# Optimization experiments

Hardware: AMD Instinct MI355X
Metric: run time of the kernel (lower is better)

Reference implementation:

```python
import jax, jax.numpy as jnp
import numpy as np

IN_SHAPE = (8, 16, 8)     # hidden_shape, prod = 1024
FF_SHAPE = (16, 16, 16)   # ff_shape, prod = 4096
RANKS = (1, 8, 8, 1)      # tt_ranks


def _make_cores(key, in_shape, out_shape, ranks):
    cores = []
    for k in range(3):
        key, sub = jax.random.split(key)
        shape = (ranks[k], in_shape[k], out_shape[k], ranks[k + 1])
        # glorot-ish scale per core
        scale = (2.0 / (in_shape[k] * ranks[k] + out_shape[k] * ranks[k + 1])) ** 0.5
        cores.append(jax.random.normal(sub, shape, dtype=jnp.float32) * scale)
    return key, cores


def setup_inputs() -> dict:
    key = jax.random.key(0)
    key, kx = jax.random.split(key)
    x = jax.random.normal(kx, (8192, int(np.prod(IN_SHAPE))), dtype=jnp.float32)
    key, c0 = _make_cores(key, IN_SHAPE, FF_SHAPE, RANKS)
    key, c1 = _make_cores(key, FF_SHAPE, IN_SHAPE, RANKS)
    b0 = jnp.zeros((int(np.prod(FF_SHAPE)),), dtype=jnp.float32)
    b1 = jnp.zeros((int(np.prod(IN_SHAPE)),), dtype=jnp.float32)
    return {
        "x": x,
        "c0a": c0[0], "c0b": c0[1], "c0c": c0[2], "b0": b0,
        "c1a": c1[0], "c1b": c1[1], "c1c": c1[2], "b1": b1,
    }


def tt_linear(x, cores, bias, in_shape, out_shape):
    # x: (B, prod(in_shape)); cores[k]: (r_k, in_k, out_k, r_{k+1})
    B = x.shape[0]
    t = x.reshape(B, *in_shape)                      # (B, i, j, k)
    t = jnp.einsum('bijk,aior->bjkor', t, cores[0])  # (B, j, k, o1, r1)
    t = jnp.einsum('bjkor,rjps->bkops', t, cores[1]) # (B, k, o1, o2, r2)
    t = jnp.einsum('bkops,skqu->bopq', t, cores[2])  # (B, o1, o2, o3)
    return t.reshape(B, -1) + bias


def reference(x, c0a, c0b, c0c, b0, c1a, c1b, c1c, b1):
    h = tt_linear(x, (c0a, c0b, c0c), b0, IN_SHAPE, FF_SHAPE)
    h = jax.nn.gelu(h, approximate=False)  # nn.GELU default = exact erf form
    out = tt_linear(h, (c1a, c1b, c1c), b1, FF_SHAPE, IN_SHAPE)
    return out
```

## Files before the change

kernel.cpp:

```cpp
#include <hip/hip_runtime.h>
#include <math.h>

typedef _Float16 f16x8 __attribute__((ext_vector_type(8)));
typedef _Float16 f16x4 __attribute__((ext_vector_type(4)));
typedef float f32x16 __attribute__((ext_vector_type(16)));

__device__ __forceinline__ void async_copy16(const void* g, void* l) {
    __builtin_amdgcn_global_load_lds(
        (const __attribute__((address_space(1))) void*)g,
        (__attribute__((address_space(3))) void*)l, 16, 0, 0);
}

__global__ __launch_bounds__(256) void cast_kernel(
    const float4* __restrict__ in, f16x4* __restrict__ out) {
    const int base = blockIdx.x * 2048 + threadIdx.x;
#pragma unroll
    for (int u = 0; u < 8; ++u) {
        float4 v = in[base + u * 256];
        f16x4 o;
        o[0] = (_Float16)v.x; o[1] = (_Float16)v.y;
        o[2] = (_Float16)v.z; o[3] = (_Float16)v.w;
        out[base + u * 256] = o;
    }
}

__global__ __launch_bounds__(256) void build_kernel(
    const float* __restrict__ c0a, const float* __restrict__ c0b,
    const float* __restrict__ c0c, _Float16* __restrict__ W0t,
    const float* __restrict__ c1a, const float* __restrict__ c1b,
    const float* __restrict__ c1c, _Float16* __restrict__ W1t) {
    __shared__ float G[16384];
    const int b = blockIdx.x, t = threadIdx.x;
    if (b < 256) {
        const int o = b >> 4, p = b & 15;
#pragma unroll
        for (int n = 0; n < 64; ++n) {
            int idx = t + 256 * n;
            int k = idx & 7, j = (idx >> 3) & 15, r = (idx >> 7) & 7, q = idx >> 10;
            float s = 0.f;
#pragma unroll
            for (int ss = 0; ss < 8; ++ss)
                s += c0b[((r * 16 + j) * 16 + p) * 8 + ss] * c0c[(ss * 8 + k) * 16 + q];
            G[idx] = s;
        }
        __syncthreads();
        const int i = t >> 5, j = (t >> 1) & 15, kq = t & 1;
        float a[8];
#pragma unroll
        for (int r = 0; r < 8; ++r) a[r] = c0a[(i * 16 + o) * 8 + r];
        const float4* G4 = (const float4*)G;
#pragma unroll
        for (int q = 0; q < 16; ++q) {
            float4 acc = {0.f, 0.f, 0.f, 0.f};
#pragma unroll
            for (int r = 0; r < 8; ++r) {
                float4 g = G4[q * 256 + r * 32 + j * 2 + kq];
                acc.x += a[r] * g.x; acc.y += a[r] * g.y;
                acc.z += a[r] * g.z; acc.w += a[r] * g.w;
            }
            f16x4 h4;
            h4[0] = (_Float16)acc.x; h4[1] = (_Float16)acc.y;
            h4[2] = (_Float16)acc.z; h4[3] = (_Float16)acc.w;
            *(f16x4*)(W0t + (size_t)((o * 16 + p) * 16 + q) * 1024 + t * 4) = h4;
        }
    } else {
        const int o = (b - 256) >> 4, p = (b - 256) & 15;
#pragma unroll
        for (int n = 0; n < 64; ++n) {
            int idx = t + 256 * n;
            int k = idx & 15, j = (idx >> 4) & 15, r = (idx >> 8) & 7, q = idx >> 11;
            float s = 0.f;
#pragma unroll
            for (int ss = 0; ss < 8; ++ss)
                s += c1b[((r * 16 + j) * 16 + p) * 8 + ss] * c1c[(ss * 16 + k) * 8 + q];
            G[idx] = s;
        }
        __syncthreads();
        const int ig = t >> 6, j = (t >> 2) & 15, kq = t & 3;
        float a[4][8];
#pragma unroll
        for (int ii = 0; ii < 4; ++ii)
#pragma unroll
            for (int r = 0; r < 8; ++r) a[ii][r] = c1a[((ig * 4 + ii) * 8 + o) * 8 + r];
        const float4* G4 = (const float4*)G;
#pragma unroll
        for (int q = 0; q < 8; ++q) {
            float4 acc[4] = {{0,0,0,0},{0,0,0,0},{0,0,0,0},{0,0,0,0}};
#pragma unroll
            for (int r = 0; r < 8; ++r) {
                float4 g = G4[q * 512 + r * 64 + j * 4 + kq];
#pragma unroll
                for (int ii = 0; ii < 4; ++ii) {
                    acc[ii].x += a[ii][r] * g.x; acc[ii].y += a[ii][r] * g.y;
                    acc[ii].z += a[ii][r] * g.z; acc[ii].w += a[ii][r] * g.w;
                }
            }
            const size_t rowbase = (size_t)((o * 16 + p) * 8 + q) * 4096;
#pragma unroll
            for (int ii = 0; ii < 4; ++ii) {
                f16x4 h4;
                h4[0] = (_Float16)acc[ii].x; h4[1] = (_Float16)acc[ii].y;
                h4[2] = (_Float16)acc[ii].z; h4[3] = (_Float16)acc[ii].w;
                *(f16x4*)(W1t + rowbase + (ig * 4 + ii) * 256 + j * 16 + kq * 4) = h4;
            }
        }
    }
}

template <int OUTMODE>
__global__ __launch_bounds__(256) void gemm32db_kernel(
    const _Float16* __restrict__ A, const _Float16* __restrict__ Bt,
    const float* __restrict__ bias, void* __restrict__ Cout,
    int M, int N, int K) {
    __shared__ alignas(16) _Float16 sA[2][8192];
    __shared__ alignas(16) _Float16 sB[2][8192];

    const int t = threadIdx.x, lane = t & 63, w = t >> 6;
    const int m0 = blockIdx.x * 128, n0 = blockIdx.y * 128;
    const int wm = (w & 1) * 64, wn = (w >> 1) * 64;
    const int l31 = lane & 31, lh = lane >> 5;
    const int fl = (l31 & 7) ^ (2 * (l31 >> 3));

    f32x16 acc[2][2] = {};

    const int s0 = w * 256 + lane;
    const int row0 = s0 >> 3;
    const int kof0 = ((lane & 7) ^ (lane >> 3)) * 8;
    const _Float16* gA = A + (size_t)(m0 + row0) * K;
    const _Float16* gB = Bt + (size_t)(n0 + row0) * K;
    const int ldst = s0 * 8;
    const size_t rs = (size_t)8 * K;

    const int nit = K >> 6;
#pragma unroll
    for (int m = 0; m < 4; ++m) {
        const int ko = kof0 ^ (16 * m);
        async_copy16(gA + m * rs + ko, &sA[0][ldst + m * 512]);
        async_copy16(gB + m * rs + ko, &sB[0][ldst + m * 512]);
    }

    for (int it = 0; it < nit; ++it) {
        __syncthreads();
        const int cur = it & 1;
        if (it + 1 < nit) {
            const int k0 = (it + 1) << 6;
#pragma unroll
            for (int m = 0; m < 4; ++m) {
                const int ko = k0 + (kof0 ^ (16 * m));
                async_copy16(gA + m * rs + ko, &sA[cur ^ 1][ldst + m * 512]);
                async_copy16(gB + m * rs + ko, &sB[cur ^ 1][ldst + m * 512]);
            }
        }
#pragma unroll
        for (int kk = 0; kk < 4; ++kk) {
            f16x8 af[2], bf[2];
            const int sl = ((kk * 2 + lh) ^ fl) * 8;
#pragma unroll
            for (int i = 0; i < 2; ++i) {
                af[i] = *(const f16x8*)(&sA[cur][(wm + i * 32 + l31) * 64 + sl]);
                bf[i] = *(const f16x8*)(&sB[cur][(wn + i * 32 + l31) * 64 + sl]);
            }
#pragma unroll
            for (int i = 0; i < 2; ++i)
#pragma unroll
                for (int j = 0; j < 2; ++j)
                    acc[i][j] = __builtin_amdgcn_mfma_f32_32x32x16_f16(af[i], bf[j], acc[i][j], 0, 0, 0);
        }
    }

#pragma unroll
    for (int i = 0; i < 2; ++i)
#pragma unroll
        for (int j = 0; j < 2; ++j) {
            const int col = n0 + wn + j * 32 + l31;
            const float bv = bias[col];
            const int rbase = m0 + wm + i * 32 + 4 * lh;
            if (OUTMODE == 1) {
                _Float16* C = (_Float16*)Cout;
#pragma unroll
                for (int r = 0; r < 16; ++r) {
                    int row = rbase + (r & 3) + 8 * (r >> 2);
                    float v = acc[i][j][r] + bv;
                    float uu = v * (0.7978845608028654f + 0.0356774081363001f * v * v);
                    float e = __builtin_amdgcn_exp2f(uu * 2.8853900817779268f);
                    float rc = __builtin_amdgcn_rcpf(e + 1.0f);
                    C[(size_t)row * N + col] = (_Float16)(v * (1.0f - rc));
                }
            } else {
                float* C = (float*)Cout;
#pragma unroll
                for (int r = 0; r < 16; ++r) {
                    int row = rbase + (r & 3) + 8 * (r >> 2);
                    C[(size_t)row * N + col] = acc[i][j][r] + bv;
                }
            }
        }
}

extern "C" void kernel_launch(void* const* d_in, const int* in_sizes, int n_in,
                              void* d_out, int out_size, void* d_ws, size_t ws_size,
                              hipStream_t stream) {
    const float* x   = (const float*)d_in[0];
    const float* c0a = (const float*)d_in[1];
    const float* c0b = (const float*)d_in[2];
    const float* c0c = (const float*)d_in[3];
    const float* b0  = (const float*)d_in[4];
    const float* c1a = (const float*)d_in[5];
    const float* c1b = (const float*)d_in[6];
    const float* c1c = (const float*)d_in[7];
    const float* b1  = (const float*)d_in[8];
    float* out = (float*)d_out;

    char* ws = (char*)d_ws;
    _Float16* xh  = (_Float16*)(ws);
    _Float16* W0t = (_Float16*)(ws + (size_t)(16u << 20));
    _Float16* W1t = (_Float16*)(ws + (size_t)(24u << 20));
    _Float16* h   = (_Float16*)(ws + (size_t)(32u << 20));

    cast_kernel<<<dim3(1024), dim3(256), 0, stream>>>((const float4*)x, (f16x4*)xh);
    build_kernel<<<dim3(384), dim3(256), 0, stream>>>(
        c0a, c0b, c0c, W0t, c1a, c1b, c1c, W1t);
    gemm32db_kernel<1><<<dim3(64, 32), dim3(256), 0, stream>>>(
        xh, W0t, b0, (void*)h, 8192, 4096, 1024);
    gemm32db_kernel<0><<<dim3(64, 8), dim3(256), 0, stream>>>(
        h, W1t, b1, (void*)out, 8192, 1024, 4096);
}
```

Measured before the change: 306.5 us.

## Drop LDS double buffering and shrink second GEMM tile to 128x64

Both GEMMs now use a single LDS buffer with load-then-sync-then-compute-then-sync, in place of double-buffered async prefetch. This halves shared memory per block so more blocks can be resident per CU. The second GEMM gets its own kernel with a 128x64 tile, which doubles the grid to 1024 blocks for better CU fill. The trade-off is lost overlap between global-to-LDS copies and MFMA within a block, relying on inter-block occupancy to hide the latency.

```diff
diff --git a/kernel.cpp b/kernel.cpp
--- a/kernel.cpp
+++ b/kernel.cpp
@@ -107,13 +107,13 @@
     }
 }
 
-template <int OUTMODE>
-__global__ __launch_bounds__(256) void gemm32db_kernel(
+__global__ __launch_bounds__(256) void gemm32_g1_kernel(
     const _Float16* __restrict__ A, const _Float16* __restrict__ Bt,
-    const float* __restrict__ bias, void* __restrict__ Cout,
+    const float* __restrict__ bias, _Float16* __restrict__ C,
     int M, int N, int K) {
-    __shared__ alignas(16) _Float16 sA[2][8192];
-    __shared__ alignas(16) _Float16 sB[2][8192];
+    constexpr int BK = 64;
+    __shared__ alignas(16) _Float16 sA[128 * BK];
+    __shared__ alignas(16) _Float16 sB[128 * BK];
 
     const int t = threadIdx.x, lane = t & 63, w = t >> 6;
     const int m0 = blockIdx.x * 128, n0 = blockIdx.y * 128;
@@ -128,37 +128,26 @@
     const int kof0 = ((lane & 7) ^ (lane >> 3)) * 8;
     const _Float16* gA = A + (size_t)(m0 + row0) * K;
     const _Float16* gB = Bt + (size_t)(n0 + row0) * K;
-    const int ldst = s0 * 8;
+    _Float16* lA = sA + s0 * 8;
+    _Float16* lB = sB + s0 * 8;
     const size_t rs = (size_t)8 * K;
 
-    const int nit = K >> 6;
-#pragma unroll
-    for (int m = 0; m < 4; ++m) {
-        const int ko = kof0 ^ (16 * m);
-        async_copy16(gA + m * rs + ko, &sA[0][ldst + m * 512]);
-        async_copy16(gB + m * rs + ko, &sB[0][ldst + m * 512]);
-    }
-
-    for (int it = 0; it < nit; ++it) {
-        __syncthreads();
-        const int cur = it & 1;
-        if (it + 1 < nit) {
-            const int k0 = (it + 1) << 6;
-#pragma unroll
-            for (int m = 0; m < 4; ++m) {
-                const int ko = k0 + (kof0 ^ (16 * m));
-                async_copy16(gA + m * rs + ko, &sA[cur ^ 1][ldst + m * 512]);
-                async_copy16(gB + m * rs + ko, &sB[cur ^ 1][ldst + m * 512]);
-            }
-        }
+    for (int k0 = 0; k0 < K; k0 += BK) {
+#pragma unroll
+        for (int m = 0; m < 4; ++m) {
+            const int ko = k0 + (kof0 ^ (16 * m));
+            async_copy16(gA + m * rs + ko, lA + m * 512);
+            async_copy16(gB + m * rs + ko, lB + m * 512);
+        }
+        __syncthreads();
 #pragma unroll
         for (int kk = 0; kk < 4; ++kk) {
             f16x8 af[2], bf[2];
             const int sl = ((kk * 2 + lh) ^ fl) * 8;
 #pragma unroll
             for (int i = 0; i < 2; ++i) {
-                af[i] = *(const f16x8*)(&sA[cur][(wm + i * 32 + l31) * 64 + sl]);
-                bf[i] = *(const f16x8*)(&sB[cur][(wn + i * 32 + l31) * 64 + sl]);
+                af[i] = *(const f16x8*)(&sA[(wm + i * 32 + l31) * 64 + sl]);
+                bf[i] = *(const f16x8*)(&sB[(wn + i * 32 + l31) * 64 + sl]);
             }
 #pragma unroll
             for (int i = 0; i < 2; ++i)
@@ -166,6 +155,7 @@
                 for (int j = 0; j < 2; ++j)
                     acc[i][j] = __builtin_amdgcn_mfma_f32_32x32x16_f16(af[i], bf[j], acc[i][j], 0, 0, 0);
         }
+        __syncthreads();
     }
 
 #pragma unroll
@@ -175,26 +165,79 @@
             const int col = n0 + wn + j * 32 + l31;
             const float bv = bias[col];
             const int rbase = m0 + wm + i * 32 + 4 * lh;
-            if (OUTMODE == 1) {
-                _Float16* C = (_Float16*)Cout;
-#pragma unroll
-                for (int r = 0; r < 16; ++r) {
-                    int row = rbase + (r & 3) + 8 * (r >> 2);
-                    float v = acc[i][j][r] + bv;
-                    float uu = v * (0.7978845608028654f + 0.0356774081363001f * v * v);
-                    float e = __builtin_amdgcn_exp2f(uu * 2.8853900817779268f);
-                    float rc = __builtin_amdgcn_rcpf(e + 1.0f);
-                    C[(size_t)row * N + col] = (_Float16)(v * (1.0f - rc));
-                }
-            } else {
-                float* C = (float*)Cout;
-#pragma unroll
-                for (int r = 0; r < 16; ++r) {
-                    int row = rbase + (r & 3) + 8 * (r >> 2);
-                    C[(size_t)row * N + col] = acc[i][j][r] + bv;
-                }
-            }
-        }
+#pragma unroll
+            for (int r = 0; r < 16; ++r) {
+                int row = rbase + (r & 3) + 8 * (r >> 2);
+                float v = acc[i][j][r] + bv;
+                float uu = v * (0.7978845608028654f + 0.0356774081363001f * v * v);
+                float e = __builtin_amdgcn_exp2f(uu * 2.8853900817779268f);
+                float rc = __builtin_amdgcn_rcpf(e + 1.0f);
+                C[(size_t)row * N + col] = (_Float16)(v * (1.0f - rc));
+            }
+        }
+}
+
+__global__ __launch_bounds__(256) void gemm32_g2_kernel(
+    const _Float16* __restrict__ A, const _Float16* __restrict__ Bt,
+    const float* __restrict__ bias, float* __restrict__ C,
+    int M, int N, int K) {
+    __shared__ alignas(16) _Float16 sA[8192];
+    __shared__ alignas(16) _Float16 sB[4096];
+
+    const int t = threadIdx.x, lane = t & 63, w = t >> 6;
+    const int m0 = blockIdx.x * 128, n0 = blockIdx.y * 64;
+    const int wm = (w & 1) * 64, wn = (w >> 1) * 32;
+    const int l31 = lane & 31, lh = lane >> 5;
+    const int fl = (l31 & 7) ^ (2 * (l31 >> 3));
+
+    f32x16 acc[2] = {};
+
+    const int s0 = w * 256 + lane;
+    const int rowA0 = s0 >> 3;
+    const int kofA = ((lane & 7) ^ (lane >> 3)) * 8;
+    const _Float16* gA = A + (size_t)(m0 + rowA0) * K;
+    _Float16* lA = sA + s0 * 8;
+    const size_t rsA = (size_t)8 * K;
+
+    const int rowB0 = t >> 3;
+    const int kofB = ((t & 7) ^ ((t >> 3) & 7) ^ (2 * (t >> 6))) * 8;
+    const _Float16* gB = Bt + (size_t)(n0 + rowB0) * K;
+    _Float16* lB = sB + t * 8;
+    const size_t rsB = (size_t)32 * K;
+
+    for (int k0 = 0; k0 < K; k0 += 64) {
+#pragma unroll
+        for (int m = 0; m < 4; ++m)
+            async_copy16(gA + m * rsA + k0 + (kofA ^ (16 * m)), lA + m * 512);
+        async_copy16(gB + k0 + kofB, lB);
+        async_copy16(gB + rsB + k0 + kofB, lB + 2048);
+        __syncthreads();
+#pragma unroll
+        for (int kk = 0; kk < 4; ++kk) {
+            f16x8 af[2], bf;
+            const int sl = ((kk * 2 + lh) ^ fl) * 8;
+#pragma unroll
+            for (int i = 0; i < 2; ++i)
+                af[i] = *(const f16x8*)(&sA[(wm + i * 32 + l31) * 64 + sl]);
+            bf = *(const f16x8*)(&sB[(wn + l31) * 64 + sl]);
+#pragma unroll
+            for (int i = 0; i < 2; ++i)
+                acc[i] = __builtin_amdgcn_mfma_f32_32x32x16_f16(af[i], bf, acc[i], 0, 0, 0);
+        }
+        __syncthreads();
+    }
+
+#pragma unroll
+    for (int i = 0; i < 2; ++i) {
+        const int col = n0 + wn + l31;
+        const float bv = bias[col];
+        const int rbase = m0 + wm + i * 32 + 4 * lh;
+#pragma unroll
+        for (int r = 0; r < 16; ++r) {
+            int row = rbase + (r & 3) + 8 * (r >> 2);
+            C[(size_t)row * N + col] = acc[i][r] + bv;
+        }
+    }
 }
 
 extern "C" void kernel_launch(void* const* d_in, const int* in_sizes, int n_in,
@@ -220,8 +263,8 @@
     cast_kernel<<<dim3(1024), dim3(256), 0, stream>>>((const float4*)x, (f16x4*)xh);
     build_kernel<<<dim3(384), dim3(256), 0, stream>>>(
         c0a, c0b, c0c, W0t, c1a, c1b, c1c, W1t);
-    gemm32db_kernel<1><<<dim3(64, 32), dim3(256), 0, stream>>>(
-        xh, W0t, b0, (void*)h, 8192, 4096, 1024);
-    gemm32db_kernel<0><<<dim3(64, 8), dim3(256), 0, stream>>>(
-        h, W1t, b1, (void*)out, 8192, 1024, 4096);
-}
+    gemm32_g1_kernel<<<dim3(64, 32), dim3(256), 0, stream>>>(
+        xh, W0t, b0, h, 8192, 4096, 1024);
+    gemm32_g2_kernel<<<dim3(64, 16), dim3(256), 0, stream>>>(
+        h, W1t, b1, out, 8192, 1024, 4096);
+}
```

Result: no change. 311.1 us (+1.5%).
